# Kernel tuning notes

Measured on AMD Instinct MI355X. Metric: run time of the kernel, lower is better.

## Reference

```python
import jax, jax.numpy as jnp
import numpy as np

B, L, H, FUTURE = 256, 1000, 51, 100


def setup_inputs() -> dict:
    key = jax.random.key(0)
    ks = jax.random.split(key, 11)
    s = 1.0 / np.sqrt(H)
    return {
        "x": jax.random.normal(ks[0], (B, L), dtype=jnp.float32),
        "W_ih1": jax.random.uniform(ks[1], (4 * H, 1), jnp.float32, -s, s),
        "W_hh1": jax.random.uniform(ks[2], (4 * H, H), jnp.float32, -s, s),
        "b_ih1": jax.random.uniform(ks[3], (4 * H,), jnp.float32, -s, s),
        "b_hh1": jax.random.uniform(ks[4], (4 * H,), jnp.float32, -s, s),
        "W_ih2": jax.random.uniform(ks[5], (4 * H, H), jnp.float32, -s, s),
        "W_hh2": jax.random.uniform(ks[6], (4 * H, H), jnp.float32, -s, s),
        "b_ih2": jax.random.uniform(ks[7], (4 * H,), jnp.float32, -s, s),
        "b_hh2": jax.random.uniform(ks[8], (4 * H,), jnp.float32, -s, s),
        "W_lin": jax.random.uniform(ks[9], (1, H), jnp.float32, -s, s),
        "b_lin": jax.random.uniform(ks[10], (1,), jnp.float32, -s, s),
        "future": FUTURE,
    }


def _lstm_cell(x_t, h, c, W_ih, W_hh, b):
    # PyTorch LSTMCell gate order: i, f, g, o
    gates = x_t @ W_ih.T + h @ W_hh.T + b  # [B, 4H]
    i, f, g, o = jnp.split(gates, 4, axis=-1)
    c_new = jax.nn.sigmoid(f) * c + jax.nn.sigmoid(i) * jnp.tanh(g)
    h_new = jax.nn.sigmoid(o) * jnp.tanh(c_new)
    return h_new, c_new


def reference(x, W_ih1, W_hh1, b_ih1, b_hh1, W_ih2, W_hh2, b_ih2, b_hh2,
              W_lin, b_lin, future):
    b1 = b_ih1 + b_hh1
    b2 = b_ih2 + b_hh2
    n, hs = x.shape[0], W_hh1.shape[1]
    zeros = jnp.zeros((n, hs), dtype=x.dtype)

    def cell_step(carry, x_t):
        h1, c1, h2, c2 = carry
        h1, c1 = _lstm_cell(x_t, h1, c1, W_ih1, W_hh1, b1)
        h2, c2 = _lstm_cell(h1, h2, c2, W_ih2, W_hh2, b2)
        out = h2 @ W_lin.T + b_lin  # [B, 1]
        return (h1, c1, h2, c2), out

    xs = x.T[:, :, None]  # [L, B, 1]
    carry, outs_seq = jax.lax.scan(cell_step, (zeros, zeros, zeros, zeros), xs)

    def future_step(carry, _):
        h1, c1, h2, c2, out = carry
        (h1, c1, h2, c2), new_out = cell_step((h1, c1, h2, c2), out)
        return (h1, c1, h2, c2, new_out), new_out

    last = outs_seq[-1]
    _, outs_fut = jax.lax.scan(future_step, (*carry, last), None, length=future)

    outs = jnp.concatenate([outs_seq, outs_fut], axis=0)  # [L+F, B, 1]
    return outs[:, :, 0].T  # [B, L+F]
```

## Files before the change

### kernel.cpp

```cpp
#include <hip/hip_runtime.h>


#define B_   256
#define L_   1000
#define H_   51
#define HP   52
#define G4   204
#define GP   208
#define T_   1100
#define NQ   13

__device__ __forceinline__ float frcp(float v) { return __builtin_amdgcn_rcpf(v); }
__device__ __forceinline__ float sigf(float v) {
    return frcp(1.0f + __expf(-v));
}
__device__ __forceinline__ float tanh_fast(float v) {
    float a = fminf(fmaxf(v, -9.0f), 9.0f);
    float e = __expf(2.0f * a);
    return (e - 1.0f) * frcp(e + 1.0f);
}

__global__ __launch_bounds__(768, 3)
void lstm_pred_kernel(const float* __restrict__ x,
                      const float* __restrict__ W_ih1, const float* __restrict__ W_hh1,
                      const float* __restrict__ b_ih1, const float* __restrict__ b_hh1,
                      const float* __restrict__ W_ih2, const float* __restrict__ W_hh2,
                      const float* __restrict__ b_ih2, const float* __restrict__ b_hh2,
                      const float* __restrict__ W_lin, const float* __restrict__ b_lin,
                      float* __restrict__ out)
{
    __shared__ float xrow[L_];
    __shared__ alignas(16) float gall[3 * GP];
    __shared__ alignas(16) float hs[2][HP];
    __shared__ float out_s;

    const int tid = threadIdx.x;
    const int b   = blockIdx.x;
    const int g   = tid >> 8;
    const int j   = tid & 255;
    const bool act = (j < G4);
    const int s   = (g == 2) ? 1 : 0;

    for (int i = tid; i < L_; i += 768) xrow[i] = x[(size_t)b * L_ + i];
    if (tid < HP) { hs[0][tid] = 0.0f; hs[1][tid] = 0.0f; }

    const float* wrow = (g == 0) ? (W_hh1 + j * H_)
                      : (g == 1) ? (W_ih2 + j * H_)
                                 : (W_hh2 + j * H_);
    float bias = 0.0f;
    float4 wA[NQ];
    if (act) {
        if (g == 0)      bias = b_ih1[j] + b_hh1[j];
        else if (g == 1) bias = b_ih2[j] + b_hh2[j];
#pragma unroll
        for (int q = 0; q < NQ; ++q) {
            wA[q].x = (4*q+0 < H_) ? wrow[4*q+0] : 0.0f;
            wA[q].y = (4*q+1 < H_) ? wrow[4*q+1] : 0.0f;
            wA[q].z = (4*q+2 < H_) ? wrow[4*q+2] : 0.0f;
            wA[q].w = (4*q+3 < H_) ? wrow[4*q+3] : 0.0f;
        }
    } else {
#pragma unroll
        for (int q = 0; q < NQ; ++q) wA[q] = make_float4(0.f, 0.f, 0.f, 0.f);
    }
    float* gdst = gall + g * GP + j;

    float wi0 = 0.f, wi1 = 0.f, wi2 = 0.f, wi3 = 0.f, wlin = 0.f;
    if (tid < H_) {
        wi0 = W_ih1[tid];
        wi1 = W_ih1[tid + H_];
        wi2 = W_ih1[tid + 2 * H_];
        wi3 = W_ih1[tid + 3 * H_];
    }
    if (tid >= 256 && tid < 256 + H_) wlin = W_lin[tid - 256];
    const float blin = b_lin[0];

    float c1 = 0.f, c2 = 0.f;
    float* outp = out + (size_t)b * T_;

    if (g == 0 && act) gall[j] = bias;
    __syncthreads();
    if (tid < H_) {
        const float xv = xrow[0];
        float gi = fmaf(wi0, xv, gall[tid]);
        float gf = fmaf(wi1, xv, gall[tid + H_]);
        float gg = fmaf(wi2, xv, gall[tid + 2 * H_]);
        float go = fmaf(wi3, xv, gall[tid + 3 * H_]);
        float ig = sigf(gi), fg = sigf(gf), gv = tanh_fast(gg), og = sigf(go);
        c1 = fmaf(fg, c1, ig * gv);
        hs[0][tid] = og * tanh_fast(c1);
    }
    __syncthreads();

    for (int t = 0; t < L_ - 1; ++t) {
        if (act) {
            const float4* h4 = (const float4*)hs[s];
            float a0 = bias, a1 = 0.f, a2 = 0.f, a3 = 0.f;
#pragma unroll
            for (int q = 0; q < NQ; ++q) {
                float4 hv = h4[q];
                a0 = fmaf(wA[q].x, hv.x, a0);
                a1 = fmaf(wA[q].y, hv.y, a1);
                a2 = fmaf(wA[q].z, hv.z, a2);
                a3 = fmaf(wA[q].w, hv.w, a3);
            }
            gdst[0] = (a0 + a1) + (a2 + a3);
        }
        __syncthreads();

        if (tid >= 256 && tid < 320) {
            float p = 0.f;
            const int q2 = tid - 256;
            if (q2 < H_) {
                float gi = gall[GP + q2]          + gall[2*GP + q2];
                float gf = gall[GP + q2 +   H_]   + gall[2*GP + q2 +   H_];
                float gg = gall[GP + q2 + 2*H_]   + gall[2*GP + q2 + 2*H_];
                float go = gall[GP + q2 + 3*H_]   + gall[2*GP + q2 + 3*H_];
                float ig = sigf(gi), fg = sigf(gf), gv = tanh_fast(gg), og = sigf(go);
                c2 = fmaf(fg, c2, ig * gv);
                float h2n = og * tanh_fast(c2);
                hs[1][q2] = h2n;
                p = h2n * wlin;
            }
#pragma unroll
            for (int off = 32; off > 0; off >>= 1) p += __shfl_down(p, off);
            if (q2 == 0) { float o = p + blin; out_s = o; outp[t] = o; }
        }
        if (tid < H_) {
            const float xv = xrow[t + 1];
            float gi = fmaf(wi0, xv, gall[tid]);
            float gf = fmaf(wi1, xv, gall[tid + H_]);
            float gg = fmaf(wi2, xv, gall[tid + 2 * H_]);
            float go = fmaf(wi3, xv, gall[tid + 3 * H_]);
            float ig = sigf(gi), fg = sigf(gf), gv = tanh_fast(gg), og = sigf(go);
            c1 = fmaf(fg, c1, ig * gv);
            hs[0][tid] = og * tanh_fast(c1);
        }
        __syncthreads();
    }

    for (int t = L_ - 1; t < T_; ++t) {
        if (act) {
            const float4* h4 = (const float4*)hs[s];
            float a0 = bias, a1 = 0.f, a2 = 0.f, a3 = 0.f;
#pragma unroll
            for (int q = 0; q < NQ; ++q) {
                float4 hv = h4[q];
                a0 = fmaf(wA[q].x, hv.x, a0);
                a1 = fmaf(wA[q].y, hv.y, a1);
                a2 = fmaf(wA[q].z, hv.z, a2);
                a3 = fmaf(wA[q].w, hv.w, a3);
            }
            gdst[0] = (a0 + a1) + (a2 + a3);
        }
        __syncthreads();

        if (tid >= 256 && tid < 320) {
            float p = 0.f;
            const int q2 = tid - 256;
            if (q2 < H_) {
                float gi = gall[GP + q2]          + gall[2*GP + q2];
                float gf = gall[GP + q2 +   H_]   + gall[2*GP + q2 +   H_];
                float gg = gall[GP + q2 + 2*H_]   + gall[2*GP + q2 + 2*H_];
                float go = gall[GP + q2 + 3*H_]   + gall[2*GP + q2 + 3*H_];
                float ig = sigf(gi), fg = sigf(gf), gv = tanh_fast(gg), og = sigf(go);
                c2 = fmaf(fg, c2, ig * gv);
                float h2n = og * tanh_fast(c2);
                hs[1][q2] = h2n;
                p = h2n * wlin;
            }
#pragma unroll
            for (int off = 32; off > 0; off >>= 1) p += __shfl_down(p, off);
            if (q2 == 0) { float o = p + blin; out_s = o; outp[t] = o; }
        }
        __syncthreads();

        if (tid < H_) {
            const float xv = out_s;
            float gi = fmaf(wi0, xv, gall[tid]);
            float gf = fmaf(wi1, xv, gall[tid + H_]);
            float gg = fmaf(wi2, xv, gall[tid + 2 * H_]);
            float go = fmaf(wi3, xv, gall[tid + 3 * H_]);
            float ig = sigf(gi), fg = sigf(gf), gv = tanh_fast(gg), og = sigf(go);
            c1 = fmaf(fg, c1, ig * gv);
            hs[0][tid] = og * tanh_fast(c1);
        }
        __syncthreads();
    }
}

extern "C" void kernel_launch(void* const* d_in, const int* in_sizes, int n_in,
                              void* d_out, int out_size, void* d_ws, size_t ws_size,
                              hipStream_t stream)
{
    const float* x     = (const float*)d_in[0];
    const float* W_ih1 = (const float*)d_in[1];
    const float* W_hh1 = (const float*)d_in[2];
    const float* b_ih1 = (const float*)d_in[3];
    const float* b_hh1 = (const float*)d_in[4];
    const float* W_ih2 = (const float*)d_in[5];
    const float* W_hh2 = (const float*)d_in[6];
    const float* b_ih2 = (const float*)d_in[7];
    const float* b_hh2 = (const float*)d_in[8];
    const float* W_lin = (const float*)d_in[9];
    const float* b_lin = (const float*)d_in[10];
    float* out = (float*)d_out;

    lstm_pred_kernel<<<B_, 768, 0, stream>>>(x, W_ih1, W_hh1, b_ih1, b_hh1,
                                             W_ih2, W_hh2, b_ih2, b_hh2,
                                             W_lin, b_lin, out);
}
```

Baseline: 1.008 ms.

## Move recurrent weight matrices from registers into transposed LDS storage

Each gate row's weights, previously held in 52 registers per thread, are now stored once per block in shared memory, transposed to column-major so that consecutive threads read consecutive addresses. This frees registers, but adds one LDS load per multiply-add in the serial matvec, and the roughly 125KB of LDS per block limits residency to one block per CU. The x row is also read directly from global memory each step instead of being staged in LDS. The extra LDS traffic on the critical recurrent path is likely to cost more than the register savings return.

```diff
diff --git a/kernel.cpp b/kernel.cpp
--- a/kernel.cpp
+++ b/kernel.cpp
@@ -6,9 +6,9 @@
 #define H_   51
 #define HP   52
 #define G4   204
-#define GP   208
 #define T_   1100
-#define NQ   13
+#define KW   (H_ * G4)
+#define SM_FLOATS (3*KW + 3*G4 + 2*HP + 4)
 
 __device__ __forceinline__ float frcp(float v) { return __builtin_amdgcn_rcpf(v); }
 __device__ __forceinline__ float sigf(float v) {
@@ -19,6 +19,26 @@
     float e = __expf(2.0f * a);
     return (e - 1.0f) * frcp(e + 1.0f);
 }
+
+#define DOTQ(q, hv) do { \
+    a0 = fmaf(wc[(4*(q)+0)*G4], (hv).x, a0); \
+    a1 = fmaf(wc[(4*(q)+1)*G4], (hv).y, a1); \
+    a2 = fmaf(wc[(4*(q)+2)*G4], (hv).z, a2); \
+    a3 = fmaf(wc[(4*(q)+3)*G4], (hv).w, a3); } while (0)
+
+#define MATVEC() do { \
+    const float4* h4 = (const float4*)hsrc; \
+    float4 v0 = h4[0], v1 = h4[1], v2 = h4[2], v3 = h4[3]; \
+    float4 v4 = h4[4], v5 = h4[5], v6 = h4[6], v7 = h4[7]; \
+    float4 v8 = h4[8], v9 = h4[9], v10 = h4[10], v11 = h4[11], v12 = h4[12]; \
+    float a0 = bias, a1 = 0.f, a2 = 0.f, a3 = 0.f; \
+    DOTQ(0, v0);  DOTQ(1, v1);  DOTQ(2, v2);  DOTQ(3, v3); \
+    DOTQ(4, v4);  DOTQ(5, v5);  DOTQ(6, v6);  DOTQ(7, v7); \
+    DOTQ(8, v8);  DOTQ(9, v9);  DOTQ(10, v10); DOTQ(11, v11); \
+    a0 = fmaf(wc[48*G4], v12.x, a0); \
+    a1 = fmaf(wc[49*G4], v12.y, a1); \
+    a2 = fmaf(wc[50*G4], v12.z, a2); \
+    gdst[0] = (a0 + a1) + (a2 + a3); } while (0)
 
 __global__ __launch_bounds__(768, 3)
 void lstm_pred_kernel(const float* __restrict__ x,
@@ -29,41 +49,42 @@
                       const float* __restrict__ W_lin, const float* __restrict__ b_lin,
                       float* __restrict__ out)
 {
-    __shared__ float xrow[L_];
-    __shared__ alignas(16) float gall[3 * GP];
-    __shared__ alignas(16) float hs[2][HP];
-    __shared__ float out_s;
+    extern __shared__ float smem[];
+    float* Wlds  = smem;
+    float* gall  = smem + 3 * KW;
+    float* hs0   = gall + 3 * G4;
+    float* hs1   = hs0 + HP;
+    float* out_p = hs1 + HP;
 
     const int tid = threadIdx.x;
     const int b   = blockIdx.x;
     const int g   = tid >> 8;
     const int j   = tid & 255;
     const bool act = (j < G4);
-    const int s   = (g == 2) ? 1 : 0;
-
-    for (int i = tid; i < L_; i += 768) xrow[i] = x[(size_t)b * L_ + i];
-    if (tid < HP) { hs[0][tid] = 0.0f; hs[1][tid] = 0.0f; }
-
-    const float* wrow = (g == 0) ? (W_hh1 + j * H_)
-                      : (g == 1) ? (W_ih2 + j * H_)
-                                 : (W_hh2 + j * H_);
+
+    {
+        const float* srcs[3] = { W_hh1, W_ih2, W_hh2 };
+#pragma unroll
+        for (int m = 0; m < 3; ++m) {
+            const float* S = srcs[m];
+            float* D = Wlds + m * KW;
+            for (int i = tid; i < KW; i += 768) {
+                int r = i / H_;
+                int k = i - r * H_;
+                D[k * G4 + r] = S[i];
+            }
+        }
+    }
+    if (tid < HP) { hs0[tid] = 0.0f; hs1[tid] = 0.0f; }
+
     float bias = 0.0f;
-    float4 wA[NQ];
     if (act) {
         if (g == 0)      bias = b_ih1[j] + b_hh1[j];
         else if (g == 1) bias = b_ih2[j] + b_hh2[j];
-#pragma unroll
-        for (int q = 0; q < NQ; ++q) {
-            wA[q].x = (4*q+0 < H_) ? wrow[4*q+0] : 0.0f;
-            wA[q].y = (4*q+1 < H_) ? wrow[4*q+1] : 0.0f;
-            wA[q].z = (4*q+2 < H_) ? wrow[4*q+2] : 0.0f;
-            wA[q].w = (4*q+3 < H_) ? wrow[4*q+3] : 0.0f;
-        }
-    } else {
-#pragma unroll
-        for (int q = 0; q < NQ; ++q) wA[q] = make_float4(0.f, 0.f, 0.f, 0.f);
-    }
-    float* gdst = gall + g * GP + j;
+    }
+    const float* wc   = Wlds + g * KW + j;
+    const float* hsrc = (g == 2) ? hs1 : hs0;
+    float* gdst = gall + g * G4 + j;
 
     float wi0 = 0.f, wi1 = 0.f, wi2 = 0.f, wi3 = 0.f, wlin = 0.f;
     if (tid < H_) {
@@ -74,6 +95,7 @@
     }
     if (tid >= 256 && tid < 256 + H_) wlin = W_lin[tid - 256];
     const float blin = b_lin[0];
+    const float* xg  = x + (size_t)b * L_;
 
     float c1 = 0.f, c2 = 0.f;
     float* outp = out + (size_t)b * T_;
@@ -81,109 +103,85 @@
     if (g == 0 && act) gall[j] = bias;
     __syncthreads();
     if (tid < H_) {
-        const float xv = xrow[0];
+        const float xv = xg[0];
         float gi = fmaf(wi0, xv, gall[tid]);
         float gf = fmaf(wi1, xv, gall[tid + H_]);
         float gg = fmaf(wi2, xv, gall[tid + 2 * H_]);
         float go = fmaf(wi3, xv, gall[tid + 3 * H_]);
         float ig = sigf(gi), fg = sigf(gf), gv = tanh_fast(gg), og = sigf(go);
         c1 = fmaf(fg, c1, ig * gv);
-        hs[0][tid] = og * tanh_fast(c1);
+        hs0[tid] = og * tanh_fast(c1);
     }
     __syncthreads();
 
     for (int t = 0; t < L_ - 1; ++t) {
-        if (act) {
-            const float4* h4 = (const float4*)hs[s];
-            float a0 = bias, a1 = 0.f, a2 = 0.f, a3 = 0.f;
-#pragma unroll
-            for (int q = 0; q < NQ; ++q) {
-                float4 hv = h4[q];
-                a0 = fmaf(wA[q].x, hv.x, a0);
-                a1 = fmaf(wA[q].y, hv.y, a1);
-                a2 = fmaf(wA[q].z, hv.z, a2);
-                a3 = fmaf(wA[q].w, hv.w, a3);
-            }
-            gdst[0] = (a0 + a1) + (a2 + a3);
-        }
+        const float xnext = xg[t + 1];
+        if (act) MATVEC();
         __syncthreads();
 
         if (tid >= 256 && tid < 320) {
             float p = 0.f;
             const int q2 = tid - 256;
             if (q2 < H_) {
-                float gi = gall[GP + q2]          + gall[2*GP + q2];
-                float gf = gall[GP + q2 +   H_]   + gall[2*GP + q2 +   H_];
-                float gg = gall[GP + q2 + 2*H_]   + gall[2*GP + q2 + 2*H_];
-                float go = gall[GP + q2 + 3*H_]   + gall[2*GP + q2 + 3*H_];
+                float gi = gall[G4 + q2]        + gall[2*G4 + q2];
+                float gf = gall[G4 + q2 +   H_] + gall[2*G4 + q2 +   H_];
+                float gg = gall[G4 + q2 + 2*H_] + gall[2*G4 + q2 + 2*H_];
+                float go = gall[G4 + q2 + 3*H_] + gall[2*G4 + q2 + 3*H_];
                 float ig = sigf(gi), fg = sigf(gf), gv = tanh_fast(gg), og = sigf(go);
                 c2 = fmaf(fg, c2, ig * gv);
                 float h2n = og * tanh_fast(c2);
-                hs[1][q2] = h2n;
+                hs1[q2] = h2n;
                 p = h2n * wlin;
             }
 #pragma unroll
             for (int off = 32; off > 0; off >>= 1) p += __shfl_down(p, off);
-            if (q2 == 0) { float o = p + blin; out_s = o; outp[t] = o; }
+            if (q2 == 0) outp[t] = p + blin;
         }
         if (tid < H_) {
-            const float xv = xrow[t + 1];
+            float gi = fmaf(wi0, xnext, gall[tid]);
+            float gf = fmaf(wi1, xnext, gall[tid + H_]);
+            float gg = fmaf(wi2, xnext, gall[tid + 2 * H_]);
+            float go = fmaf(wi3, xnext, gall[tid + 3 * H_]);
+            float ig = sigf(gi), fg = sigf(gf), gv = tanh_fast(gg), og = sigf(go);
+            c1 = fmaf(fg, c1, ig * gv);
+            hs0[tid] = og * tanh_fast(c1);
+        }
+        __syncthreads();
+    }
+
+    for (int t = L_ - 1; t < T_; ++t) {
+        if (act) MATVEC();
+        __syncthreads();
+
+        if (tid >= 256 && tid < 320) {
+            float p = 0.f;
+            const int q2 = tid - 256;
+            if (q2 < H_) {
+                float gi = gall[G4 + q2]        + gall[2*G4 + q2];
+                float gf = gall[G4 + q2 +   H_] + gall[2*G4 + q2 +   H_];
+                float gg = gall[G4 + q2 + 2*H_] + gall[2*G4 + q2 + 2*H_];
+                float go = gall[G4 + q2 + 3*H_] + gall[2*G4 + q2 + 3*H_];
+                float ig = sigf(gi), fg = sigf(gf), gv = tanh_fast(gg), og = sigf(go);
+                c2 = fmaf(fg, c2, ig * gv);
+                float h2n = og * tanh_fast(c2);
+                hs1[q2] = h2n;
+                p = h2n * wlin;
+            }
+#pragma unroll
+            for (int off = 32; off > 0; off >>= 1) p += __shfl_down(p, off);
+            if (q2 == 0) { float o = p + blin; *out_p = o; outp[t] = o; }
+        }
+        __syncthreads();
+
+        if (tid < H_) {
+            const float xv = *out_p;
             float gi = fmaf(wi0, xv, gall[tid]);
             float gf = fmaf(wi1, xv, gall[tid + H_]);
             float gg = fmaf(wi2, xv, gall[tid + 2 * H_]);
             float go = fmaf(wi3, xv, gall[tid + 3 * H_]);
             float ig = sigf(gi), fg = sigf(gf), gv = tanh_fast(gg), og = sigf(go);
             c1 = fmaf(fg, c1, ig * gv);
-            hs[0][tid] = og * tanh_fast(c1);
-        }
-        __syncthreads();
-    }
-
-    for (int t = L_ - 1; t < T_; ++t) {
-        if (act) {
-            const float4* h4 = (const float4*)hs[s];
-            float a0 = bias, a1 = 0.f, a2 = 0.f, a3 = 0.f;
-#pragma unroll
-            for (int q = 0; q < NQ; ++q) {
-                float4 hv = h4[q];
-                a0 = fmaf(wA[q].x, hv.x, a0);
-                a1 = fmaf(wA[q].y, hv.y, a1);
-                a2 = fmaf(wA[q].z, hv.z, a2);
-                a3 = fmaf(wA[q].w, hv.w, a3);
-            }
-            gdst[0] = (a0 + a1) + (a2 + a3);
-        }
-        __syncthreads();
-
-        if (tid >= 256 && tid < 320) {
-            float p = 0.f;
-            const int q2 = tid - 256;
-            if (q2 < H_) {
-                float gi = gall[GP + q2]          + gall[2*GP + q2];
-                float gf = gall[GP + q2 +   H_]   + gall[2*GP + q2 +   H_];
-                float gg = gall[GP + q2 + 2*H_]   + gall[2*GP + q2 + 2*H_];
-                float go = gall[GP + q2 + 3*H_]   + gall[2*GP + q2 + 3*H_];
-                float ig = sigf(gi), fg = sigf(gf), gv = tanh_fast(gg), og = sigf(go);
-                c2 = fmaf(fg, c2, ig * gv);
-                float h2n = og * tanh_fast(c2);
-                hs[1][q2] = h2n;
-                p = h2n * wlin;
-            }
-#pragma unroll
-            for (int off = 32; off > 0; off >>= 1) p += __shfl_down(p, off);
-            if (q2 == 0) { float o = p + blin; out_s = o; outp[t] = o; }
-        }
-        __syncthreads();
-
-        if (tid < H_) {
-            const float xv = out_s;
-            float gi = fmaf(wi0, xv, gall[tid]);
-            float gf = fmaf(wi1, xv, gall[tid + H_]);
-            float gg = fmaf(wi2, xv, gall[tid + 2 * H_]);
-            float go = fmaf(wi3, xv, gall[tid + 3 * H_]);
-            float ig = sigf(gi), fg = sigf(gf), gv = tanh_fast(gg), og = sigf(go);
-            c1 = fmaf(fg, c1, ig * gv);
-            hs[0][tid] = og * tanh_fast(c1);
+            hs0[tid] = og * tanh_fast(c1);
         }
         __syncthreads();
     }
@@ -206,7 +204,16 @@
     const float* b_lin = (const float*)d_in[10];
     float* out = (float*)d_out;
 
-    lstm_pred_kernel<<<B_, 768, 0, stream>>>(x, W_ih1, W_hh1, b_ih1, b_hh1,
-                                             W_ih2, W_hh2, b_ih2, b_hh2,
-                                             W_lin, b_lin, out);
-}
+    const size_t smem_bytes = SM_FLOATS * sizeof(float);
+    static bool attr_set = false;
+    if (!attr_set) {
+        (void)hipFuncSetAttribute((const void*)lstm_pred_kernel,
+                                  hipFuncAttributeMaxDynamicSharedMemorySize,
+                                  (int)smem_bytes);
+        attr_set = true;
+    }
+
+    lstm_pred_kernel<<<B_, 768, smem_bytes, stream>>>(x, W_ih1, W_hh1, b_ih1, b_hh1,
+                                                      W_ih2, W_hh2, b_ih2, b_hh2,
+                                                      W_lin, b_lin, out);
+}
```

New measurement: 1.559 ms. 1.55x slower.
